# Kernel tuning notes

Measured on AMD Instinct MI355X. Metric: run time of the kernel, lower is better.

## Reference

```python
import jax, jax.numpy as jnp
import numpy as np

N = 50000
E = 1600000
IN_CH = 128
HID = 32
HEADS = 4
NEG_SLOPE = 0.2
BN_EPS = 1e-5


def _gat_layer(x, src, dst, W, att_src, att_dst, n):
    """PyG-style GATConv (no bias; bias added by caller).
    x: [n, f_in], W: [f_in, heads*out], att_*: [heads, out].
    Returns [n, heads, out]."""
    heads, out_ch = att_src.shape
    h = (x @ W).reshape(n, heads, out_ch)                 # node projections
    a_s = jnp.einsum('nhc,hc->nh', h, att_src)            # per-node src logit
    a_d = jnp.einsum('nhc,hc->nh', h, att_dst)            # per-node dst logit
    e = jax.nn.leaky_relu(a_s[src] + a_d[dst], NEG_SLOPE)  # [E_tot, heads]
    m = jax.ops.segment_max(e, dst, num_segments=n)       # per-target max (stable softmax)
    ex = jnp.exp(e - m[dst])
    denom = jax.ops.segment_sum(ex, dst, num_segments=n)
    alpha = ex / denom[dst]                               # segment softmax over incoming edges
    out = jax.ops.segment_sum(h[src] * alpha[:, :, None], dst, num_segments=n)
    return out


def setup_inputs():
    key = jax.random.key(0)
    ks = jax.random.split(key, 8)
    x = jax.random.normal(ks[0], (N, IN_CH), dtype=jnp.float32)
    edge_index = jax.random.randint(ks[1], (2, E), 0, N, dtype=jnp.int32)
    s1 = 1.0 / float(np.sqrt(IN_CH))
    W1 = jax.random.uniform(ks[2], (IN_CH, HEADS * HID), jnp.float32, -s1, s1)
    att_src1 = jax.random.uniform(ks[3], (HEADS, HID), jnp.float32, -s1, s1)
    att_dst1 = jax.random.uniform(ks[4], (HEADS, HID), jnp.float32, -s1, s1)
    bias1 = jnp.zeros((HEADS * HID,), jnp.float32)
    bn_gamma = jnp.ones((HEADS * HID,), jnp.float32)
    bn_beta = jnp.zeros((HEADS * HID,), jnp.float32)
    bn_mean = jnp.zeros((HEADS * HID,), jnp.float32)
    bn_var = jnp.ones((HEADS * HID,), jnp.float32)
    s2 = 1.0 / float(np.sqrt(HEADS * HID))
    W2 = jax.random.uniform(ks[5], (HEADS * HID, 2), jnp.float32, -s2, s2)
    att_src2 = jax.random.uniform(ks[6], (1, 2), jnp.float32, -s2, s2)
    att_dst2 = jax.random.uniform(ks[7], (1, 2), jnp.float32, -s2, s2)
    bias2 = jnp.zeros((2,), jnp.float32)
    return {"x": x, "edge_index": edge_index, "W1": W1, "att_src1": att_src1,
            "att_dst1": att_dst1, "bias1": bias1, "bn_gamma": bn_gamma,
            "bn_beta": bn_beta, "bn_mean": bn_mean, "bn_var": bn_var,
            "W2": W2, "att_src2": att_src2, "att_dst2": att_dst2, "bias2": bias2}


def reference(x, edge_index, W1, att_src1, att_dst1, bias1, bn_gamma, bn_beta,
              bn_mean, bn_var, W2, att_src2, att_dst2, bias2):
    n = x.shape[0]
    # PyG GATConv default add_self_loops=True
    loop = jnp.arange(n, dtype=edge_index.dtype)
    src = jnp.concatenate([edge_index[0], loop])
    dst = jnp.concatenate([edge_index[1], loop])
    # conv1 (concat=True) + bias
    h1 = _gat_layer(x, src, dst, W1, att_src1, att_dst1, n).reshape(n, -1) + bias1
    # BatchNorm1d (eval mode, running stats)
    h1 = bn_gamma * (h1 - bn_mean) / jnp.sqrt(bn_var + BN_EPS) + bn_beta
    h1 = jax.nn.leaky_relu(h1, NEG_SLOPE)
    # dropout is identity in eval mode
    # conv2 (heads=1, concat=False -> mean over heads) + bias
    h2 = _gat_layer(h1, src, dst, W2, att_src2, att_dst2, n).mean(axis=1) + bias2
    return jax.nn.log_softmax(h2, axis=1)
```

## Files before the change

kernel.cpp:

```cpp
#include <hip/hip_runtime.h>
#include <math.h>

#define NN 50000
#define EE 1600000
#define FIN 128
#define FOUT 128
#define NEG 0.2f
#define BNEPS 1e-5f

#define NPART 8
#define PSZ (NN / NPART)

#define SCB 49
#define BEB 1024
#define NBUCK ((EE + BEB - 1) / BEB)
#define GGRP 8
#define BCAPG 30000
#define DSUB 8

#define XS_STRIDE 132
__global__ __launch_bounds__(256) void k_proj(const float* __restrict__ x,
    const float* __restrict__ W1, const float* __restrict__ asw, const float* __restrict__ adw,
    signed char* __restrict__ h8, float* __restrict__ hscale,
    float* __restrict__ as1, float* __restrict__ ad1) {
  __shared__ float xs[64 * XS_STRIDE];
  int t = threadIdx.x;
  int nb = blockIdx.x * 64;

  #pragma unroll
  for (int j = 0; j < 8; ++j) {
    int idx = t + 256 * j;
    int r = idx >> 5;
    int c4 = idx & 31;
    int n = nb + r; if (n >= NN) n = NN - 1;
    float4 v = *(const float4*)(x + (size_t)n * FIN + c4 * 4);
    *(float4*)(&xs[r * XS_STRIDE + c4 * 4]) = v;
  }
  __syncthreads();

  int cg = t & 15;
  int ng = t >> 4;
  int c0 = cg * 8;

  float acc[4][8];
  #pragma unroll
  for (int i = 0; i < 4; ++i)
    #pragma unroll
    for (int j = 0; j < 8; ++j) acc[i][j] = 0.f;

  for (int k0 = 0; k0 < FIN; k0 += 4) {
    float xr[4][4];
    #pragma unroll
    for (int i = 0; i < 4; ++i)
      *(float4*)xr[i] = *(const float4*)&xs[(ng * 4 + i) * XS_STRIDE + k0];
    #pragma unroll
    for (int kk = 0; kk < 4; ++kk) {
      float4 w0 = *(const float4*)(W1 + (k0 + kk) * FOUT + c0);
      float4 w1 = *(const float4*)(W1 + (k0 + kk) * FOUT + c0 + 4);
      float wv[8] = {w0.x, w0.y, w0.z, w0.w, w1.x, w1.y, w1.z, w1.w};
      #pragma unroll
      for (int i = 0; i < 4; ++i) {
        float xv = xr[i][kk];
        #pragma unroll
        for (int j = 0; j < 8; ++j) acc[i][j] = fmaf(xv, wv[j], acc[i][j]);
      }
    }
  }

  int head = cg >> 2;
  float vs[4], vd[4], rmax[4];
  #pragma unroll
  for (int i = 0; i < 4; ++i) {
    float s = 0.f, d = 0.f, m = 0.f;
    #pragma unroll
    for (int j = 0; j < 8; ++j) {
      s = fmaf(acc[i][j], asw[c0 + j], s);
      d = fmaf(acc[i][j], adw[c0 + j], d);
      m = fmaxf(m, fabsf(acc[i][j]));
    }
    vs[i] = s; vd[i] = d; rmax[i] = m;
  }
  #pragma unroll
  for (int i = 0; i < 4; ++i) {
    rmax[i] = fmaxf(rmax[i], __shfl_xor(rmax[i], 1, 64));
    rmax[i] = fmaxf(rmax[i], __shfl_xor(rmax[i], 2, 64));
    rmax[i] = fmaxf(rmax[i], __shfl_xor(rmax[i], 4, 64));
    rmax[i] = fmaxf(rmax[i], __shfl_xor(rmax[i], 8, 64));
  }
  #pragma unroll
  for (int i = 0; i < 4; ++i) {
    int n = nb + ng * 4 + i;
    if (n >= NN) continue;
    float rm = fmaxf(rmax[i], 1e-30f);
    float inv = 127.f / rm;
    unsigned b[8];
    #pragma unroll
    for (int j = 0; j < 8; ++j) {
      float qf = fminf(127.f, fmaxf(-127.f, rintf(acc[i][j] * inv)));
      b[j] = (unsigned)((int)qf) & 0xffu;
    }
    uint2 pk;
    pk.x = b[0] | (b[1] << 8) | (b[2] << 16) | (b[3] << 24);
    pk.y = b[4] | (b[5] << 8) | (b[6] << 16) | (b[7] << 24);
    *(uint2*)(h8 + (size_t)n * FOUT + c0) = pk;
    if (cg == 0) hscale[n] = rm / 127.f;
  }
  #pragma unroll
  for (int i = 0; i < 4; ++i) {
    vs[i] += __shfl_xor(vs[i], 1, 64); vs[i] += __shfl_xor(vs[i], 2, 64);
    vd[i] += __shfl_xor(vd[i], 1, 64); vd[i] += __shfl_xor(vd[i], 2, 64);
  }
  if ((cg & 3) == 0) {
    #pragma unroll
    for (int i = 0; i < 4; ++i) {
      int n = nb + ng * 4 + i;
      if (n < NN) { as1[n * 4 + head] = vs[i]; ad1[n * 4 + head] = vd[i]; }
    }
  }
}

__global__ __launch_bounds__(256) void k_bucket(const int* __restrict__ ei,
    int* __restrict__ bcur, unsigned* __restrict__ bkt) {
  __shared__ int lcnt[NPART];
  __shared__ int gbase[NPART];
  int t = threadIdx.x;
  int g = blockIdx.x & (GGRP - 1);
  if (t < NPART) lcnt[t] = 0;
  __syncthreads();
  int e0 = blockIdx.x * BEB;
  int part[4]; int lslot[4]; unsigned pk[4];
  #pragma unroll
  for (int j = 0; j < 4; ++j) {
    int i = e0 + j * 256 + t;
    if (i < EE) {
      int s = ei[i];
      int d = ei[EE + i];
      int p = d / PSZ;
      part[j] = p;
      pk[j] = (unsigned)s | ((unsigned)(d - p * PSZ) << 17);
      lslot[j] = atomicAdd(&lcnt[p], 1);
    } else part[j] = -1;
  }
  __syncthreads();
  if (t < NPART) gbase[t] = atomicAdd(&bcur[(g * NPART + t) * 16], lcnt[t]);
  __syncthreads();
  #pragma unroll
  for (int j = 0; j < 4; ++j) {
    if (part[j] >= 0)
      bkt[(size_t)(g * NPART + part[j]) * BCAPG + gbase[part[j]] + lslot[j]] = pk[j];
  }
}

__global__ __launch_bounds__(1024) void k_deg(const int* __restrict__ bcur,
    const unsigned* __restrict__ bkt, int* __restrict__ degp) {
  __shared__ int lh[PSZ];
  int t = threadIdx.x;
  int part = blockIdx.x & (NPART - 1);
  int g    = blockIdx.x >> 3;
  for (int i = t; i < PSZ; i += 1024) lh[i] = 0;
  __syncthreads();
  int cnt = bcur[(g * NPART + part) * 16];
  const unsigned* b = bkt + (size_t)(g * NPART + part) * BCAPG;
  for (int i = t; i < cnt; i += 1024)
    atomicAdd(&lh[b[i] >> 17], 1);
  __syncthreads();
  int* dst = degp + ((size_t)part * DSUB + g) * PSZ;
  for (int i = t; i < PSZ; i += 1024) dst[i] = lh[i];
}

__global__ __launch_bounds__(1024) void k_scanA(const int* __restrict__ degp,
    int* __restrict__ cur, int* __restrict__ bsum) {
  __shared__ int sums[1024];
  int t = threadIdx.x;
  int idx = blockIdx.x * 1024 + t;
  int v = 0;
  if (idx < NN) {
    int p = idx / PSZ, l = idx - p * PSZ;
    v = 1;
    #pragma unroll
    for (int k = 0; k < DSUB; ++k)
      v += degp[((size_t)p * DSUB + k) * PSZ + l];
  }
  sums[t] = v; __syncthreads();
  #pragma unroll
  for (int off = 1; off < 1024; off <<= 1) {
    int u = (t >= off) ? sums[t - off] : 0;
    __syncthreads();
    sums[t] += u;
    __syncthreads();
  }
  if (idx < NN) cur[idx] = sums[t] - v;
  if (t == 1023) bsum[blockIdx.x] = sums[1023];
}

__global__ __launch_bounds__(1024) void k_scanB(const int* __restrict__ bsum,
    int* __restrict__ offs, int* __restrict__ cur) {
  int b = blockIdx.x;
  int t = threadIdx.x;
  int base = 0;
  for (int i = 0; i < SCB; ++i) base += (i < b) ? bsum[i] : 0;
  int idx = b * 1024 + t;
  if (idx < NN) {
    int v = cur[idx] + base;
    offs[idx] = v;
    cur[idx] = v;
  }
  if (b == SCB - 1 && t == 0) {
    int total = base;
    for (int i = b; i < SCB; ++i) total += bsum[i];
    offs[NN] = total;
  }
}

__global__ __launch_bounds__(1024) void k_scat3(const int* __restrict__ bcur,
    const unsigned* __restrict__ bkt, const int* __restrict__ offs,
    const int* __restrict__ degp, int* __restrict__ csr) {
  __shared__ int lcur[PSZ];
  int t = threadIdx.x;
  int p = blockIdx.x & (NPART - 1);
  int g = blockIdx.x >> 3;
  int nbase = p * PSZ;
  for (int i = t; i < PSZ; i += 1024) {
    int c = offs[nbase + i];
    for (int gp = 0; gp < g; ++gp)
      c += degp[((size_t)p * DSUB + gp) * PSZ + i];
    lcur[i] = c;
  }
  __syncthreads();
  int cnt = bcur[(g * NPART + p) * 16];
  const unsigned* b = bkt + (size_t)(g * NPART + p) * BCAPG;
  for (int i = t; i < cnt; i += 1024) {
    unsigned v = b[i];
    int pos = atomicAdd(&lcur[v >> 17], 1);
    csr[pos] = (int)(v & 0x1ffffu);
  }
  if (g == DSUB - 1) {
    __syncthreads();
    for (int i = t; i < PSZ; i += 1024)
      csr[lcur[i]] = nbase + i;
  }
}

__global__ __launch_bounds__(256) void k_agg1(
    const int* __restrict__ offs, const int* __restrict__ csr,
    const signed char* __restrict__ h8, const float* __restrict__ hscale,
    const float* __restrict__ as1, const float* __restrict__ ad1,
    const float* __restrict__ bias1, const float* __restrict__ gamma, const float* __restrict__ beta,
    const float* __restrict__ mean, const float* __restrict__ var,
    const float* __restrict__ W2, const float* __restrict__ asw2, const float* __restrict__ adw2,
    float* __restrict__ h2, float* __restrict__ as2, float* __restrict__ ad2) {
  __shared__ int   slds[4][32];
  __shared__ float wlds[4][32][4];
  int wid = threadIdx.x >> 6;
  int lane = threadIdx.x & 63;
  int n = blockIdx.x * 4 + wid;
  if (n >= NN) return;
  int r0 = offs[n], r1 = offs[n + 1];
  int l  = lane & 31;
  int hf = lane >> 5;
  int hh = l >> 3;
  const signed char* hpb = h8;
  float2 adv = *(const float2*)(ad1 + n * 4 + hf * 2);

  float acc0 = 0.f, acc1 = 0.f, acc2 = 0.f, acc3 = 0.f;
  float denp0 = 0.f, denp1 = 0.f;

#define AGG_PRE(IDX, PRED)                                         \
  {                                                                \
    int sv = csr[(IDX)];                                           \
    float hs = hscale[sv];                                         \
    float2 av = *(const float2*)(as1 + sv * 4 + hf * 2);           \
    float e0 = av.x + adv.x; e0 = e0 > 0.f ? e0 : NEG * e0;        \
    float e1 = av.y + adv.y; e1 = e1 > 0.f ? e1 : NEG * e1;        \
    float ex0 = __expf(e0), ex1 = __expf(e1);                      \
    float w0 = ex0 * hs, w1 = ex1 * hs;                            \
    if (PRED) { denp0 += ex0; denp1 += ex1; }                      \
    wlds[wid][l][hf * 2]     = (PRED) ? w0 : 0.f;                  \
    wlds[wid][l][hf * 2 + 1] = (PRED) ? w1 : 0.f;                  \
    if (hf == 0) slds[wid][l] = sv;                                \
  }

#define AGG_BODY(J)                                                \
  {                                                                \
    int s = slds[wid][hf * 16 + (J)];                              \
    float w = wlds[wid][hf * 16 + (J)][hh];                        \
    unsigned pv = *(const unsigned*)(hpb + (size_t)s * FOUT + l * 4); \
    int q0 = ((int)(pv << 24)) >> 24;                              \
    int q1 = ((int)(pv << 16)) >> 24;                              \
    int q2 = ((int)(pv << 8)) >> 24;                               \
    int q3 = ((int)pv) >> 24;                                      \
    acc0 = fmaf(w, (float)q0, acc0);                               \
    acc1 = fmaf(w, (float)q1, acc1);                               \
    acc2 = fmaf(w, (float)q2, acc2);                               \
    acc3 = fmaf(w, (float)q3, acc3);                               \
  }

  int base = r0;
  for (; base + 32 <= r1; base += 32) {
    AGG_PRE(base + l, true)
    #pragma unroll
    for (int j = 0; j < 16; ++j) AGG_BODY(j)
  }
  int m = r1 - base;
  if (m > 0) {
    AGG_PRE(base + (l < m ? l : m - 1), l < m)
    int jmax = m < 16 ? m : 16;
    for (int j = 0; j < jmax; ++j) AGG_BODY(j)
  }

  acc0 += __shfl_xor(acc0, 32, 64);
  acc1 += __shfl_xor(acc1, 32, 64);
  acc2 += __shfl_xor(acc2, 32, 64);
  acc3 += __shfl_xor(acc3, 32, 64);

  #pragma unroll
  for (int mm = 16; mm >= 1; mm >>= 1) {
    denp0 += __shfl_xor(denp0, mm, 64);
    denp1 += __shfl_xor(denp1, mm, 64);
  }
  float dOA = __shfl_xor(denp0, 32, 64);
  float dOB = __shfl_xor(denp1, 32, 64);
  float den0 = hf ? dOA : denp0;
  float den1 = hf ? dOB : denp1;
  float den2 = hf ? denp0 : dOA;
  float den3 = hf ? denp1 : dOB;
  float den = (hh == 0) ? den0 : (hh == 1) ? den1 : (hh == 2) ? den2 : den3;

  int c0 = l * 4;
  float inv = 1.f / den;
  float4 bi = *(const float4*)(bias1 + c0);
  float4 ga = *(const float4*)(gamma + c0);
  float4 be = *(const float4*)(beta + c0);
  float4 mu = *(const float4*)(mean + c0);
  float4 va = *(const float4*)(var + c0);
  float o0 = acc0 * inv + bi.x;
  float o1 = acc1 * inv + bi.y;
  float o2 = acc2 * inv + bi.z;
  float o3 = acc3 * inv + bi.w;
  o0 = ga.x * (o0 - mu.x) * rsqrtf(va.x + BNEPS) + be.x;
  o1 = ga.y * (o1 - mu.y) * rsqrtf(va.y + BNEPS) + be.y;
  o2 = ga.z * (o2 - mu.z) * rsqrtf(va.z + BNEPS) + be.z;
  o3 = ga.w * (o3 - mu.w) * rsqrtf(va.w + BNEPS) + be.w;
  o0 = o0 > 0.f ? o0 : NEG * o0;
  o1 = o1 > 0.f ? o1 : NEG * o1;
  o2 = o2 > 0.f ? o2 : NEG * o2;
  o3 = o3 > 0.f ? o3 : NEG * o3;

  float p0 = o0 * W2[(c0 + 0) * 2 + 0] + o1 * W2[(c0 + 1) * 2 + 0]
           + o2 * W2[(c0 + 2) * 2 + 0] + o3 * W2[(c0 + 3) * 2 + 0];
  float p1 = o0 * W2[(c0 + 0) * 2 + 1] + o1 * W2[(c0 + 1) * 2 + 1]
           + o2 * W2[(c0 + 2) * 2 + 1] + o3 * W2[(c0 + 3) * 2 + 1];
  #pragma unroll
  for (int mm = 16; mm >= 1; mm >>= 1) {
    p0 += __shfl_xor(p0, mm, 64);
    p1 += __shfl_xor(p1, mm, 64);
  }
  if (lane == 0) {
    h2[n * 2 + 0] = p0;
    h2[n * 2 + 1] = p1;
    as2[n] = p0 * asw2[0] + p1 * asw2[1];
    ad2[n] = p0 * adw2[0] + p1 * adw2[1];
  }
}

__global__ __launch_bounds__(256) void k_agg2(
    const int* __restrict__ offs, const int* __restrict__ csr,
    const float* __restrict__ h2, const float* __restrict__ as2, const float* __restrict__ ad2,
    const float* __restrict__ bias2, float* __restrict__ out) {
  int wid = threadIdx.x >> 6;
  int lane = threadIdx.x & 63;
  int n = blockIdx.x * 4 + wid;
  if (n >= NN) return;
  int r0 = offs[n], r1 = offs[n + 1];
  float ad = ad2[n];

  float den = 0.f, a0 = 0.f, a1 = 0.f;
  for (int i = r0 + lane; i < r1; i += 64) {
    int s = csr[i];
    float e = as2[s] + ad; e = e > 0.f ? e : NEG * e;
    float ex = __expf(e);
    float2 hv = *(const float2*)(h2 + s * 2);
    den += ex;
    a0 = fmaf(ex, hv.x, a0);
    a1 = fmaf(ex, hv.y, a1);
  }
  #pragma unroll
  for (int mm = 32; mm >= 1; mm >>= 1) {
    den += __shfl_xor(den, mm, 64);
    a0  += __shfl_xor(a0, mm, 64);
    a1  += __shfl_xor(a1, mm, 64);
  }
  if (lane == 0) {
    float o0 = a0 / den + bias2[0];
    float o1 = a1 / den + bias2[1];
    float mx = fmaxf(o0, o1);
    float lse = mx + logf(__expf(o0 - mx) + __expf(o1 - mx));
    out[n * 2 + 0] = o0 - lse;
    out[n * 2 + 1] = o1 - lse;
  }
}

extern "C" void kernel_launch(void* const* d_in, const int* in_sizes, int n_in,
                              void* d_out, int out_size, void* d_ws, size_t ws_size,
                              hipStream_t stream) {
  const float* x     = (const float*)d_in[0];
  const int*   ei    = (const int*)d_in[1];
  const float* W1    = (const float*)d_in[2];
  const float* asw1  = (const float*)d_in[3];
  const float* adw1  = (const float*)d_in[4];
  const float* bias1 = (const float*)d_in[5];
  const float* gamma = (const float*)d_in[6];
  const float* beta  = (const float*)d_in[7];
  const float* mean  = (const float*)d_in[8];
  const float* var   = (const float*)d_in[9];
  const float* W2    = (const float*)d_in[10];
  const float* asw2  = (const float*)d_in[11];
  const float* adw2  = (const float*)d_in[12];
  const float* bias2 = (const float*)d_in[13];
  float* out = (float*)d_out;

  char* ws = (char*)d_ws;
  size_t off = 0;
  auto alloc = [&](size_t bytes) {
    void* p = ws + off;
    off += (bytes + 255) & ~(size_t)255;
    return p;
  };
  signed char* h8 = (signed char*)alloc((size_t)NN * FOUT);
  float* hscale = (float*)alloc((size_t)NN * 4);
  float* as1  = (float*)alloc((size_t)NN * 4 * 4);
  float* ad1  = (float*)alloc((size_t)NN * 4 * 4);
  int*   degp = (int*)alloc((size_t)NPART * DSUB * PSZ * 4);
  int*   offs = (int*)alloc(((size_t)NN + 1) * 4);
  int*   cur  = (int*)alloc((size_t)NN * 4);
  int*   bsum = (int*)alloc((size_t)SCB * 4);
  int*   bcur = (int*)alloc((size_t)GGRP * NPART * 16 * 4);
  int*   csr  = (int*)alloc((size_t)(EE + NN) * 4);
  unsigned* bkt = (unsigned*)alloc((size_t)GGRP * NPART * BCAPG * 4);
  float* h2   = (float*)alloc((size_t)NN * 2 * 4);
  float* as2  = (float*)alloc((size_t)NN * 4);
  float* ad2  = (float*)alloc((size_t)NN * 4);
  (void)ws_size; (void)in_sizes; (void)n_in; (void)out_size;

  hipMemsetAsync(bcur, 0, (size_t)GGRP * NPART * 16 * 4, stream);
  k_proj   <<<(NN + 63) / 64, 256, 0, stream>>>(x, W1, asw1, adw1, h8, hscale, as1, ad1);
  k_bucket <<<NBUCK, 256, 0, stream>>>(ei, bcur, bkt);
  k_deg    <<<NPART * DSUB, 1024, 0, stream>>>(bcur, bkt, degp);
  k_scanA  <<<SCB, 1024, 0, stream>>>(degp, cur, bsum);
  k_scanB  <<<SCB, 1024, 0, stream>>>(bsum, offs, cur);
  k_scat3  <<<NPART * DSUB, 1024, 0, stream>>>(bcur, bkt, offs, degp, csr);
  k_agg1   <<<(NN + 3) / 4, 256, 0, stream>>>(offs, csr, h8, hscale, as1, ad1, bias1, gamma, beta,
                                              mean, var, W2, asw2, adw2, h2, as2, ad2);
  k_agg2   <<<(NN + 3) / 4, 256, 0, stream>>>(offs, csr, h2, as2, ad2, bias2, out);
}
```

Measured before the change: 169.4 us.

## Fuse CSR scans into scatter kernel, store x as bf16 in LDS, pack agg LDS

Merges the two scan kernels and the scatter kernel into one kernel. Each block recomputes its partition's offsets from the bucket counts and degree histograms, which removes two launches and the cur/bsum round trips. The projection kernel now stores x in shared memory as bf16, halving LDS footprint and read traffic at the cost of input precision. The aggregation kernel packs source index and weight into one uint2 LDS entry so each step does a single LDS read instead of two.

```diff
diff --git a/kernel.cpp b/kernel.cpp
--- a/kernel.cpp
+++ b/kernel.cpp
@@ -11,19 +11,24 @@
 #define NPART 8
 #define PSZ (NN / NPART)
 
-#define SCB 49
 #define BEB 1024
 #define NBUCK ((EE + BEB - 1) / BEB)
 #define GGRP 8
 #define BCAPG 30000
 #define DSUB 8
 
-#define XS_STRIDE 132
+static __device__ __forceinline__ unsigned f2bf(float f) {
+  unsigned int u = __float_as_uint(f);
+  u += 0x7fffu + ((u >> 16) & 1u);
+  return u >> 16;
+}
+
+#define XSS 66
 __global__ __launch_bounds__(256) void k_proj(const float* __restrict__ x,
     const float* __restrict__ W1, const float* __restrict__ asw, const float* __restrict__ adw,
     signed char* __restrict__ h8, float* __restrict__ hscale,
     float* __restrict__ as1, float* __restrict__ ad1) {
-  __shared__ float xs[64 * XS_STRIDE];
+  __shared__ unsigned xs[64 * XSS];
   int t = threadIdx.x;
   int nb = blockIdx.x * 64;
 
@@ -34,7 +39,8 @@
     int c4 = idx & 31;
     int n = nb + r; if (n >= NN) n = NN - 1;
     float4 v = *(const float4*)(x + (size_t)n * FIN + c4 * 4);
-    *(float4*)(&xs[r * XS_STRIDE + c4 * 4]) = v;
+    xs[r * XSS + c4 * 2]     = f2bf(v.x) | (f2bf(v.y) << 16);
+    xs[r * XSS + c4 * 2 + 1] = f2bf(v.z) | (f2bf(v.w) << 16);
   }
   __syncthreads();
 
@@ -51,8 +57,13 @@
   for (int k0 = 0; k0 < FIN; k0 += 4) {
     float xr[4][4];
     #pragma unroll
-    for (int i = 0; i < 4; ++i)
-      *(float4*)xr[i] = *(const float4*)&xs[(ng * 4 + i) * XS_STRIDE + k0];
+    for (int i = 0; i < 4; ++i) {
+      uint2 u = *(const uint2*)&xs[(ng * 4 + i) * XSS + (k0 >> 1)];
+      xr[i][0] = __uint_as_float(u.x << 16);
+      xr[i][1] = __uint_as_float(u.x & 0xffff0000u);
+      xr[i][2] = __uint_as_float(u.y << 16);
+      xr[i][3] = __uint_as_float(u.y & 0xffff0000u);
+    }
     #pragma unroll
     for (int kk = 0; kk < 4; ++kk) {
       float4 w0 = *(const float4*)(W1 + (k0 + kk) * FOUT + c0);
@@ -168,66 +179,64 @@
   for (int i = t; i < PSZ; i += 1024) dst[i] = lh[i];
 }
 
-__global__ __launch_bounds__(1024) void k_scanA(const int* __restrict__ degp,
-    int* __restrict__ cur, int* __restrict__ bsum) {
+__global__ __launch_bounds__(1024) void k_scat4(const int* __restrict__ bcur,
+    const unsigned* __restrict__ bkt, const int* __restrict__ degp,
+    int* __restrict__ offs, int* __restrict__ csr) {
+  __shared__ int lcur[PSZ];
   __shared__ int sums[1024];
+  __shared__ int sb[GGRP * NPART];
   int t = threadIdx.x;
-  int idx = blockIdx.x * 1024 + t;
-  int v = 0;
-  if (idx < NN) {
-    int p = idx / PSZ, l = idx - p * PSZ;
-    v = 1;
-    #pragma unroll
-    for (int k = 0; k < DSUB; ++k)
-      v += degp[((size_t)p * DSUB + k) * PSZ + l];
-  }
-  sums[t] = v; __syncthreads();
-  #pragma unroll
+  int p = blockIdx.x & (NPART - 1);
+  int g = blockIdx.x >> 3;
+  if (t < GGRP * NPART) sb[t] = bcur[t * 16];
+  __syncthreads();
+
+  int base_p = 0;
+  for (int pp = 0; pp < p; ++pp) {
+    int s = PSZ;
+    for (int gg = 0; gg < GGRP; ++gg) s += sb[gg * NPART + pp];
+    base_p += s;
+  }
+
+  const int CH = 7;
+  int n0 = t * CH;
+  int tsum = 0;
+  for (int i = 0; i < CH; ++i) {
+    int idx = n0 + i;
+    if (idx < PSZ) {
+      int v = 1;
+      for (int gg = 0; gg < GGRP; ++gg)
+        v += degp[((size_t)p * DSUB + gg) * PSZ + idx];
+      tsum += v;
+    }
+  }
+  sums[t] = tsum; __syncthreads();
   for (int off = 1; off < 1024; off <<= 1) {
     int u = (t >= off) ? sums[t - off] : 0;
     __syncthreads();
     sums[t] += u;
     __syncthreads();
   }
-  if (idx < NN) cur[idx] = sums[t] - v;
-  if (t == 1023) bsum[blockIdx.x] = sums[1023];
-}
-
-__global__ __launch_bounds__(1024) void k_scanB(const int* __restrict__ bsum,
-    int* __restrict__ offs, int* __restrict__ cur) {
-  int b = blockIdx.x;
-  int t = threadIdx.x;
-  int base = 0;
-  for (int i = 0; i < SCB; ++i) base += (i < b) ? bsum[i] : 0;
-  int idx = b * 1024 + t;
-  if (idx < NN) {
-    int v = cur[idx] + base;
-    offs[idx] = v;
-    cur[idx] = v;
-  }
-  if (b == SCB - 1 && t == 0) {
-    int total = base;
-    for (int i = b; i < SCB; ++i) total += bsum[i];
-    offs[NN] = total;
-  }
-}
-
-__global__ __launch_bounds__(1024) void k_scat3(const int* __restrict__ bcur,
-    const unsigned* __restrict__ bkt, const int* __restrict__ offs,
-    const int* __restrict__ degp, int* __restrict__ csr) {
-  __shared__ int lcur[PSZ];
-  int t = threadIdx.x;
-  int p = blockIdx.x & (NPART - 1);
-  int g = blockIdx.x >> 3;
-  int nbase = p * PSZ;
-  for (int i = t; i < PSZ; i += 1024) {
-    int c = offs[nbase + i];
-    for (int gp = 0; gp < g; ++gp)
-      c += degp[((size_t)p * DSUB + gp) * PSZ + i];
-    lcur[i] = c;
-  }
-  __syncthreads();
-  int cnt = bcur[(g * NPART + p) * 16];
+  int run = base_p + ((t == 0) ? 0 : sums[t - 1]);
+  for (int i = 0; i < CH; ++i) {
+    int idx = n0 + i;
+    if (idx < PSZ) {
+      int v = 1, pre = 0;
+      for (int gg = 0; gg < GGRP; ++gg) {
+        int d = degp[((size_t)p * DSUB + gg) * PSZ + idx];
+        v += d;
+        if (gg < g) pre += d;
+      }
+      if (g == 0) offs[p * PSZ + idx] = run;
+      lcur[idx] = run + pre;
+      run += v;
+    }
+  }
+  if (g == 0 && p == NPART - 1 && t == 1023)
+    offs[NN] = base_p + sums[1023];
+  __syncthreads();
+
+  int cnt = sb[g * NPART + p];
   const unsigned* b = bkt + (size_t)(g * NPART + p) * BCAPG;
   for (int i = t; i < cnt; i += 1024) {
     unsigned v = b[i];
@@ -237,7 +246,7 @@
   if (g == DSUB - 1) {
     __syncthreads();
     for (int i = t; i < PSZ; i += 1024)
-      csr[lcur[i]] = nbase + i;
+      csr[lcur[i]] = p * PSZ + i;
   }
 }
 
@@ -249,8 +258,7 @@
     const float* __restrict__ mean, const float* __restrict__ var,
     const float* __restrict__ W2, const float* __restrict__ asw2, const float* __restrict__ adw2,
     float* __restrict__ h2, float* __restrict__ as2, float* __restrict__ ad2) {
-  __shared__ int   slds[4][32];
-  __shared__ float wlds[4][32][4];
+  __shared__ uint2 swlds[4][32][4];
   int wid = threadIdx.x >> 6;
   int lane = threadIdx.x & 63;
   int n = blockIdx.x * 4 + wid;
@@ -273,17 +281,18 @@
     float e0 = av.x + adv.x; e0 = e0 > 0.f ? e0 : NEG * e0;        \
     float e1 = av.y + adv.y; e1 = e1 > 0.f ? e1 : NEG * e1;        \
     float ex0 = __expf(e0), ex1 = __expf(e1);                      \
-    float w0 = ex0 * hs, w1 = ex1 * hs;                            \
     if (PRED) { denp0 += ex0; denp1 += ex1; }                      \
-    wlds[wid][l][hf * 2]     = (PRED) ? w0 : 0.f;                  \
-    wlds[wid][l][hf * 2 + 1] = (PRED) ? w1 : 0.f;                  \
-    if (hf == 0) slds[wid][l] = sv;                                \
+    float w0 = (PRED) ? ex0 * hs : 0.f;                            \
+    float w1 = (PRED) ? ex1 * hs : 0.f;                            \
+    swlds[wid][l][hf * 2]     = make_uint2((unsigned)sv, __float_as_uint(w0)); \
+    swlds[wid][l][hf * 2 + 1] = make_uint2((unsigned)sv, __float_as_uint(w1)); \
   }
 
 #define AGG_BODY(J)                                                \
   {                                                                \
-    int s = slds[wid][hf * 16 + (J)];                              \
-    float w = wlds[wid][hf * 16 + (J)][hh];                        \
+    uint2 sw = swlds[wid][hf * 16 + (J)][hh];                      \
+    int s = (int)sw.x;                                             \
+    float w = __uint_as_float(sw.y);                               \
     unsigned pv = *(const unsigned*)(hpb + (size_t)s * FOUT + l * 4); \
     int q0 = ((int)(pv << 24)) >> 24;                              \
     int q1 = ((int)(pv << 16)) >> 24;                              \
@@ -432,8 +441,6 @@
   float* ad1  = (float*)alloc((size_t)NN * 4 * 4);
   int*   degp = (int*)alloc((size_t)NPART * DSUB * PSZ * 4);
   int*   offs = (int*)alloc(((size_t)NN + 1) * 4);
-  int*   cur  = (int*)alloc((size_t)NN * 4);
-  int*   bsum = (int*)alloc((size_t)SCB * 4);
   int*   bcur = (int*)alloc((size_t)GGRP * NPART * 16 * 4);
   int*   csr  = (int*)alloc((size_t)(EE + NN) * 4);
   unsigned* bkt = (unsigned*)alloc((size_t)GGRP * NPART * BCAPG * 4);
@@ -446,9 +453,7 @@
   k_proj   <<<(NN + 63) / 64, 256, 0, stream>>>(x, W1, asw1, adw1, h8, hscale, as1, ad1);
   k_bucket <<<NBUCK, 256, 0, stream>>>(ei, bcur, bkt);
   k_deg    <<<NPART * DSUB, 1024, 0, stream>>>(bcur, bkt, degp);
-  k_scanA  <<<SCB, 1024, 0, stream>>>(degp, cur, bsum);
-  k_scanB  <<<SCB, 1024, 0, stream>>>(bsum, offs, cur);
-  k_scat3  <<<NPART * DSUB, 1024, 0, stream>>>(bcur, bkt, offs, degp, csr);
+  k_scat4  <<<NPART * DSUB, 1024, 0, stream>>>(bcur, bkt, degp, offs, csr);
   k_agg1   <<<(NN + 3) / 4, 256, 0, stream>>>(offs, csr, h8, hscale, as1, ad1, bias1, gamma, beta,
                                               mean, var, W2, asw2, adw2, h2, as2, ad2);
   k_agg2   <<<(NN + 3) / 4, 256, 0, stream>>>(offs, csr, h2, as2, ad2, bias2, out);
```

Result: slower. 193.1 us (+14.0%).
